# Performance work log

Hardware: AMD Instinct MI355X
Metric: run time of the kernel (lower is better)

Reference implementation:

```python
import jax, jax.numpy as jnp
import numpy as np

N = 50000      # nodes
E = 800000     # edges (avg degree 16)
C_IN = 128
C_HID = 256
C_OUT = 256
SLOPE = 0.2    # LeakyReLU negative slope (PyG GATv2Conv default)


def gatv2_layer(x, src, dst, edge_attr, Wl, Wr, We, att, bias):
    """PyG GATv2Conv, heads=1, share_weights=False.
    e_ij = att . leaky_relu(Wl x_j + Wr x_i + We e_ij); softmax over incoming
    edges of each target i; out_i = sum_j alpha_ij * (Wl x_j) + bias."""
    xl = x @ Wl                       # [N, out] source transform
    xr = x @ Wr                       # [N, out] target transform
    ee = edge_attr[:, None] @ We      # [E, out] edge feature transform (edge_dim=1)
    m = xl[src] + xr[dst] + ee        # [E, out] per-edge message pre-activation
    e = jnp.einsum('ed,d->e', jax.nn.leaky_relu(m, SLOPE), att)  # [E]
    # segment softmax over target nodes
    emax = jax.ops.segment_max(e, dst, num_segments=N)           # [N]
    ex = jnp.exp(e - emax[dst])                                  # [E]
    denom = jax.ops.segment_sum(ex, dst, num_segments=N)         # [N]
    alpha = ex / denom[dst]                                      # [E]
    out = jax.ops.segment_sum(xl[src] * alpha[:, None], dst, num_segments=N)
    return out + bias


def setup_inputs() -> dict:
    key = jax.random.key(0)
    ks = jax.random.split(key, 24)

    def lin(k, i, o):
        return (jax.random.normal(k, (i, o), jnp.float32) / np.sqrt(i)).astype(jnp.float32)

    inp = {
        'features': jax.random.normal(ks[0], (N, C_IN), jnp.float32),
        'edge_index': jax.random.randint(ks[1], (2, E), 0, N, dtype=jnp.int64),
        'edge_attr': jax.random.uniform(ks[2], (E,), jnp.float32),
        # conv1: c_in -> c_hidden
        'Wl1': lin(ks[3], C_IN, C_HID), 'Wr1': lin(ks[4], C_IN, C_HID),
        'We1': lin(ks[5], 1, C_HID),
        'a1': jax.random.normal(ks[6], (C_HID,), jnp.float32) / np.sqrt(C_HID),
        'bb1': jnp.zeros((C_HID,), jnp.float32),
        # conv2: c_hidden -> c_hidden
        'Wl2': lin(ks[7], C_HID, C_HID), 'Wr2': lin(ks[8], C_HID, C_HID),
        'We2': lin(ks[9], 1, C_HID),
        'a2': jax.random.normal(ks[10], (C_HID,), jnp.float32) / np.sqrt(C_HID),
        'bb2': jnp.zeros((C_HID,), jnp.float32),
        # conv3: c_hidden -> c_out (concat=False, heads=1 -> same math)
        'Wl3': lin(ks[11], C_HID, C_OUT), 'Wr3': lin(ks[12], C_HID, C_OUT),
        'We3': lin(ks[13], 1, C_OUT),
        'a3': jax.random.normal(ks[14], (C_OUT,), jnp.float32) / np.sqrt(C_OUT),
        'bb3': jnp.zeros((C_OUT,), jnp.float32),
        # MLP head: Linear(c_out,10) -> relu -> Linear(10,1); dropout is eval-mode identity
        'Wh1': lin(ks[15], C_OUT, 10), 'bh1': jnp.zeros((10,), jnp.float32),
        'Wh2': lin(ks[16], 10, 1), 'bh2': jnp.zeros((1,), jnp.float32),
    }
    return inp


def reference(features, edge_index, edge_attr,
              Wl1, Wr1, We1, a1, bb1,
              Wl2, Wr2, We2, a2, bb2,
              Wl3, Wr3, We3, a3, bb3,
              Wh1, bh1, Wh2, bh2):
    src, dst = edge_index[0], edge_index[1]
    x1 = jax.nn.relu(gatv2_layer(features, src, dst, edge_attr, Wl1, Wr1, We1, a1, bb1))
    x2 = jax.nn.relu(gatv2_layer(x1, src, dst, edge_attr, Wl2, Wr2, We2, a2, bb2))
    x3 = jax.nn.relu(gatv2_layer(x2, src, dst, edge_attr, Wl3, Wr3, We3, a3, bb3))
    x4 = jnp.max(x3, axis=-2)                 # global max pool over nodes -> [c_out]
    x5 = jax.nn.relu(x4 @ Wh1 + bh1)          # [10]
    return x5 @ Wh2 + bh2                     # [1]
```

## Files before the change

kernel.cpp:

```cpp
#include <hip/hip_runtime.h>
#include <cstddef>
#include <cstdint>

typedef __attribute__((ext_vector_type(8))) short short8v;
typedef __attribute__((ext_vector_type(4))) short short4v;
typedef __attribute__((ext_vector_type(4))) float floatx4;

__device__ __forceinline__ float b2f(short u){
    return __uint_as_float(((unsigned)(unsigned short)u) << 16);
}
__device__ __forceinline__ short f2b(float f){
    unsigned x = __float_as_uint(f);
    unsigned r = x + 0x7FFFu + ((x >> 16) & 1u);
    return (short)(r >> 16);
}
__device__ __forceinline__ float loadF(const void* p, size_t i, int isBf16){
    return isBf16 ? b2f(((const short*)p)[i]) : ((const float*)p)[i];
}
__device__ __forceinline__ int loadI(const void* p, size_t i, int isI64){
    return isI64 ? ((const int*)p)[2 * i] : ((const int*)p)[i];
}

__global__ void detect_kernel(const void* feat, const void* ei, int E, int* flags){
    int lane = threadIdx.x;
    if (lane >= 8 && lane < 16) flags[lane] = 0;
    const unsigned short* fs = (const unsigned short*)feat;
    int plaus = 0;
    for (int j = lane; j < 128; j += 64){
        unsigned short s = fs[2 * j];
        int e = (s >> 7) & 0xFF;
        if (s == 0 || (e >= 100 && e <= 140)) plaus++;
    }
    #pragma unroll
    for (int o = 32; o > 0; o >>= 1) plaus += __shfl_xor(plaus, o);
    const int* ew = (const int*)ei;
    int zeros = 0;
    for (int j = lane; j < 128; j += 64) if (ew[2 * j + 1] == 0) zeros++;
    #pragma unroll
    for (int o = 32; o > 0; o >>= 1) zeros += __shfl_xor(zeros, o);
    if (lane == 0){ flags[0] = (plaus >= 64) ? 1 : 0; flags[1] = (zeros >= 64) ? 1 : 0; }
    (void)E;
}

__global__ void sentinel_kernel(void* out, const int* flags, float v){
    if (threadIdx.x == 0){
        if (flags[0]) ((short*)out)[0] = f2b(v);
        else          ((float*)out)[0] = v;
    }
}

__global__ void zero3(int* cnt, int* fill, unsigned* pool, int N){
    int i = blockIdx.x * 256 + threadIdx.x;
    if (i < N){ cnt[i] = 0; fill[i] = 0; }
    if (i < 256) pool[i] = 0u;
}

__global__ void hist_kernel(const void* __restrict__ ei, int* __restrict__ cnt, int E,
                            const int* __restrict__ flags){
    int i = blockIdx.x * 256 + threadIdx.x;
    if (i < E) atomicAdd(&cnt[loadI(ei, (size_t)E + i, flags[1])], 1);
}

__global__ void scanA(const int* __restrict__ cnt, int* __restrict__ off,
                      int* __restrict__ partial, int N){
    __shared__ int wsum[16];
    const int t = threadIdx.x, w = t >> 6, lane = t & 63;
    int i = blockIdx.x * 1024 + t;
    int v = (i < N) ? cnt[i] : 0;
    int x = v;
    #pragma unroll
    for (int o = 1; o < 64; o <<= 1){
        int y = __shfl_up(x, o);
        if (lane >= o) x += y;
    }
    if (lane == 63) wsum[w] = x;
    __syncthreads();
    if (w == 0){
        int mv = (lane < 16) ? wsum[lane] : 0;
        int xx = mv;
        #pragma unroll
        for (int o = 1; o < 16; o <<= 1){
            int y = __shfl_up(xx, o);
            if (lane >= o) xx += y;
        }
        if (lane < 16) wsum[lane] = xx - mv;
    }
    __syncthreads();
    int incl = x + wsum[w];
    if (i < N) off[i] = incl - v;
    if (t == 1023) partial[blockIdx.x] = incl;
}

__global__ void scanB(int* __restrict__ partial, int* __restrict__ off, int nb, int N){
    int lane = threadIdx.x;
    int v = (lane < nb) ? partial[lane] : 0;
    int x = v;
    #pragma unroll
    for (int o = 1; o < 64; o <<= 1){
        int y = __shfl_up(x, o);
        if (lane >= o) x += y;
    }
    if (lane < nb) partial[lane] = x - v;
    if (lane == 63) off[N] = x;
}

__global__ void scanC(int* __restrict__ off, const int* __restrict__ partial, int N){
    int i = blockIdx.x * 1024 + threadIdx.x;
    if (i < N) off[i] += partial[blockIdx.x];
}

__global__ void scatter_kernel(const void* __restrict__ ei, const void* __restrict__ ea,
                               const int* __restrict__ off, int* __restrict__ fill,
                               int* __restrict__ srcS, float* __restrict__ eaS,
                               int E, const int* __restrict__ flags){
    int i = blockIdx.x * 256 + threadIdx.x;
    if (i >= E) return;
    int d = loadI(ei, (size_t)E + i, flags[1]);
    int pos = off[d] + atomicAdd(&fill[d], 1);
    srcS[pos] = loadI(ei, (size_t)i, flags[1]);
    eaS[pos] = loadF(ea, (size_t)i, flags[0]);
}

__global__ void prep_b(const void* __restrict__ W, short* __restrict__ bhi,
                       short* __restrict__ blo, int K, const int* __restrict__ flags,
                       int* __restrict__ hasLo){
    int idx = blockIdx.x * 256 + threadIdx.x;
    int k = idx >> 8, c = idx & 255;
    float v = loadF(W, idx, flags[0]);
    short h = f2b(v);
    short l = f2b(v - b2f(h));
    bhi[(size_t)c * K + k] = h;
    blo[(size_t)c * K + k] = l;
    if (__ballot(l != 0) != 0ull && (threadIdx.x & 63) == 0) atomicOr(hasLo, 1);
}

struct DJob { const void* src; float* dst; int n; };
struct DJobs { DJob j[13]; };
__global__ void decode_many(DJobs jobs, const int* __restrict__ flags){
    const DJob J = jobs.j[blockIdx.x];
    int fbf = flags[0];
    for (int i = threadIdx.x; i < J.n; i += 256)
        J.dst[i] = loadF(J.src, (size_t)i, fbf);
}

template<int BZ>
__global__ __launch_bounds__(256, 3) void gemm_tpl(
        const void* __restrict__ A, const short* __restrict__ Alo, int aRaw,
        const short* __restrict__ Bhi, const short* __restrict__ Blo,
        float* __restrict__ C, int M, int K,
        const int* __restrict__ flags, const int* __restrict__ bLoFlag){
    if (BZ ? (bLoFlag[0] != 0) : (bLoFlag[0] == 0)) return;
    __shared__ __align__(16) short Ah[128 * 64];
    __shared__ __align__(16) short Al[128 * 64];
    __shared__ __align__(16) short Bh[128 * 64];
    __shared__ __align__(16) short Bl[BZ ? 8 : 128 * 64];
    const int fbf = flags[0];
    const int az = (aRaw && fbf) ? 1 : 0;
    const int t = threadIdx.x;
    const int w = t >> 6, lane = t & 63;
    const int wr = w >> 1, wc = w & 1;
    const int bRow = blockIdx.x * 128;
    const int bCol = blockIdx.y * 128;

    floatx4 acc[4][4];
    #pragma unroll
    for (int m = 0; m < 4; m++)
        #pragma unroll
        for (int n = 0; n < 4; n++) acc[m][n] = (floatx4){0.f, 0.f, 0.f, 0.f};

    for (int k0 = 0; k0 < K; k0 += 64){
        #pragma unroll
        for (int i = 0; i < 4; i++){
            int e = i * 256 + t;
            int r = e >> 3, c = e & 7;
            int sw = (((c << 4) ^ ((r & 7) << 4)) >> 1);
            int gr = bRow + r; if (gr >= M) gr = M - 1;
            size_t ga = (size_t)gr * K + k0 + c * 8;
            if (aRaw){
                if (fbf){
                    *(short8v*)&Ah[r * 64 + sw] = *(const short8v*)&((const short*)A)[ga];
                } else {
                    const float* Af = (const float*)A;
                    floatx4 v0 = *(const floatx4*)&Af[ga];
                    floatx4 v1 = *(const floatx4*)&Af[ga + 4];
                    short8v h, l;
                    #pragma unroll
                    for (int j = 0; j < 4; j++){
                        short hj = f2b(v0[j]);
                        h[j] = hj; l[j] = f2b(v0[j] - b2f(hj));
                        short hk = f2b(v1[j]);
                        h[4 + j] = hk; l[4 + j] = f2b(v1[j] - b2f(hk));
                    }
                    *(short8v*)&Ah[r * 64 + sw] = h;
                    *(short8v*)&Al[r * 64 + sw] = l;
                }
            } else {
                *(short8v*)&Ah[r * 64 + sw] = *(const short8v*)&((const short*)A)[ga];
                *(short8v*)&Al[r * 64 + sw] = *(const short8v*)&Alo[ga];
            }
            size_t gb = (size_t)(bCol + r) * K + k0 + c * 8;
            *(short8v*)&Bh[r * 64 + sw] = *(const short8v*)&Bhi[gb];
            if (!BZ) *(short8v*)&Bl[r * 64 + sw] = *(const short8v*)&Blo[gb];
        }
        __syncthreads();
        #pragma unroll
        for (int ks = 0; ks < 2; ks++){
            short8v a_h[4], a_l[4], b_h[4], b_l[4];
            #pragma unroll
            for (int m = 0; m < 4; m++){
                int ar = wr * 64 + m * 16 + (lane & 15);
                int co = (((ks * 64 + ((lane >> 4) << 4)) ^ ((ar & 7) << 4)) >> 1);
                a_h[m] = *(const short8v*)&Ah[ar * 64 + co];
                if (!az) a_l[m] = *(const short8v*)&Al[ar * 64 + co];
            }
            #pragma unroll
            for (int n = 0; n < 4; n++){
                int br = wc * 64 + n * 16 + (lane & 15);
                int co = (((ks * 64 + ((lane >> 4) << 4)) ^ ((br & 7) << 4)) >> 1);
                b_h[n] = *(const short8v*)&Bh[br * 64 + co];
                if (!BZ) b_l[n] = *(const short8v*)&Bl[br * 64 + co];
            }
            #pragma unroll
            for (int m = 0; m < 4; m++)
                #pragma unroll
                for (int n = 0; n < 4; n++){
                    if (!az) acc[m][n] = __builtin_amdgcn_mfma_f32_16x16x32_bf16(
                                             a_l[m], b_h[n], acc[m][n], 0, 0, 0);
                    if (!BZ) acc[m][n] = __builtin_amdgcn_mfma_f32_16x16x32_bf16(
                                             a_h[m], b_l[n], acc[m][n], 0, 0, 0);
                    acc[m][n] = __builtin_amdgcn_mfma_f32_16x16x32_bf16(
                                    a_h[m], b_h[n], acc[m][n], 0, 0, 0);
                }
        }
        __syncthreads();
    }
    #pragma unroll
    for (int m = 0; m < 4; m++){
        int rb = bRow + wr * 64 + m * 16 + ((lane >> 4) << 2);
        #pragma unroll
        for (int n = 0; n < 4; n++){
            int cg = bCol + wc * 64 + n * 16 + (lane & 15);
            #pragma unroll
            for (int r = 0; r < 4; r++){
                int gr = rb + r;
                if (gr < M) C[(size_t)gr * 512 + cg] = acc[m][n][r];
            }
        }
    }
}

__global__ __launch_bounds__(256) void fused_agg(const float* __restrict__ PR,
        const int* __restrict__ srcS, const float* __restrict__ eaS,
        const int* __restrict__ off, const float* __restrict__ WeF,
        const float* __restrict__ attF, const float* __restrict__ bbF,
        short* __restrict__ QHi, short* __restrict__ QLo, int N){
    int node = blockIdx.x * 4 + (threadIdx.x >> 6);
    int lane = threadIdx.x & 63;
    if (node >= N) return;
    const int beg = off[node], end = off[node + 1];
    const int dd = lane << 2;
    const floatx4 xr4 = *(const floatx4*)&PR[(size_t)node * 512 + 256 + dd];
    const floatx4 we4 = *(const floatx4*)&WeF[dd];
    const floatx4 at4 = *(const floatx4*)&attF[dd];
    float m = -1e30f, ssum = 0.f;
    floatx4 a4 = (floatx4){0.f, 0.f, 0.f, 0.f};
    for (int k0 = beg; k0 < end; k0 += 8){
        floatx4 v[8]; float pp[8]; float eav[8];
        #pragma unroll
        for (int c = 0; c < 8; c++){
            int k = k0 + c; if (k >= end) k = end - 1;
            int s = srcS[k];
            eav[c] = eaS[k];
            v[c] = *(const floatx4*)&PR[(size_t)s * 512 + dd];
        }
        #pragma unroll
        for (int c = 0; c < 8; c++){
            float p = 0.f;
            #pragma unroll
            for (int j = 0; j < 4; j++){
                float tv = v[c][j] + xr4[j] + eav[c] * we4[j];
                tv = tv > 0.f ? tv : 0.2f * tv;
                p += tv * at4[j];
            }
            #pragma unroll
            for (int o = 32; o > 0; o >>= 1) p += __shfl_xor(p, o);
            pp[c] = (k0 + c < end) ? p : -1e30f;
        }
        float pm = pp[0];
        #pragma unroll
        for (int c = 1; c < 8; c++) pm = fmaxf(pm, pp[c]);
        float newm = fmaxf(m, pm);
        float scale = __expf(m - newm);
        ssum *= scale;
        a4[0] *= scale; a4[1] *= scale; a4[2] *= scale; a4[3] *= scale;
        #pragma unroll
        for (int c = 0; c < 8; c++){
            float wgt = __expf(pp[c] - newm);
            ssum += wgt;
            a4[0] += wgt * v[c][0]; a4[1] += wgt * v[c][1];
            a4[2] += wgt * v[c][2]; a4[3] += wgt * v[c][3];
        }
        m = newm;
    }
    float inv = (end > beg) ? 1.f / ssum : 0.f;
    short4v h4, l4;
    #pragma unroll
    for (int j = 0; j < 4; j++){
        float o = fmaxf(a4[j] * inv + bbF[dd + j], 0.f);
        short h = f2b(o);
        h4[j] = h;
        l4[j] = f2b(o - b2f(h));
    }
    *(short4v*)&QHi[(size_t)node * 256 + dd] = h4;
    *(short4v*)&QLo[(size_t)node * 256 + dd] = l4;
}

__global__ __launch_bounds__(256) void col_max2(const short* __restrict__ hi,
        const short* __restrict__ lo, unsigned* __restrict__ pool, int N){
    int lane = threadIdx.x & 63;
    int w = threadIdx.x >> 6;
    int dd = lane << 2;
    floatx4 mx = (floatx4){0.f, 0.f, 0.f, 0.f};
    for (int r = blockIdx.x * 4 + w; r < N; r += gridDim.x * 4){
        short4v h = *(const short4v*)&hi[(size_t)r * 256 + dd];
        short4v l = *(const short4v*)&lo[(size_t)r * 256 + dd];
        mx[0] = fmaxf(mx[0], b2f(h[0]) + b2f(l[0]));
        mx[1] = fmaxf(mx[1], b2f(h[1]) + b2f(l[1]));
        mx[2] = fmaxf(mx[2], b2f(h[2]) + b2f(l[2]));
        mx[3] = fmaxf(mx[3], b2f(h[3]) + b2f(l[3]));
    }
    atomicMax(&pool[dd + 0], __float_as_uint(mx[0]));
    atomicMax(&pool[dd + 1], __float_as_uint(mx[1]));
    atomicMax(&pool[dd + 2], __float_as_uint(mx[2]));
    atomicMax(&pool[dd + 3], __float_as_uint(mx[3]));
}

__global__ void head_kernel(const unsigned* __restrict__ pool, const float* __restrict__ Wh1F,
        const float* __restrict__ bh1F, const float* __restrict__ Wh2F,
        const float* __restrict__ bh2F, void* __restrict__ out, const int* __restrict__ flags){
    int lane = threadIdx.x;
    float acc = 0.f;
    if (lane < 10){
        acc = bh1F[lane];
        for (int d = 0; d < 256; ++d)
            acc += __uint_as_float(pool[d]) * Wh1F[d * 10 + lane];
        acc = fmaxf(acc, 0.f) * Wh2F[lane];
    }
    #pragma unroll
    for (int o = 32; o > 0; o >>= 1) acc += __shfl_xor(acc, o);
    if (lane == 0){
        float r = acc + bh2F[0];
        if (flags[0]) ((short*)out)[0] = f2b(r);
        else          ((float*)out)[0] = r;
    }
}

extern "C" void kernel_launch(void* const* d_in, const int* in_sizes, int n_in,
                              void* d_out, int out_size, void* d_ws, size_t ws_size,
                              hipStream_t stream){
    const void* feat = d_in[0];
    const void* ei   = d_in[1];
    const void* ea   = d_in[2];
    const void* Wl[3] = {d_in[3], d_in[8],  d_in[13]};
    const void* Wr[3] = {d_in[4], d_in[9],  d_in[14]};
    const void* We[3] = {d_in[5], d_in[10], d_in[15]};
    const void* at[3] = {d_in[6], d_in[11], d_in[16]};
    const void* bb[3] = {d_in[7], d_in[12], d_in[17]};
    const void* Wh1 = d_in[18];
    const void* bh1 = d_in[19];
    const void* Wh2 = d_in[20];
    const void* bh2 = d_in[21];

    const int N = in_sizes[0] / 128;
    const int E = in_sizes[1] / 2;
    const int Kin[3] = {128, 256, 256};
    const int nb = (N + 1023) / 1024;

    char* p = (char*)d_ws;
    auto alloc = [&](size_t bytes) -> void* {
        void* r = (void*)p; p += (bytes + 255) & ~(size_t)255; return r;
    };
    int*   flags   = (int*)alloc(256);
    int*   partial = (int*)alloc(256 * 4);
    int*   off   = (int*)alloc((size_t)(N + 1) * 4);
    int*   cnt   = (int*)alloc((size_t)N * 4);
    int*   fill  = (int*)alloc((size_t)N * 4);
    int*   srcS  = (int*)alloc((size_t)E * 4);
    float* eaS   = (float*)alloc((size_t)E * 4);
    float* PR    = (float*)alloc((size_t)N * 512 * 4);
    short* QHi   = (short*)alloc((size_t)N * 256 * 2);
    short* QLo   = (short*)alloc((size_t)N * 256 * 2);
    short* BtH[3]; short* BtL[3];
    for (int i = 0; i < 3; i++){
        BtH[i] = (short*)alloc((size_t)512 * Kin[i] * 2);
        BtL[i] = (short*)alloc((size_t)512 * Kin[i] * 2);
    }
    float* WeF  = (float*)alloc(3 * 256 * 4);
    float* attF = (float*)alloc(3 * 256 * 4);
    float* bbF  = (float*)alloc(3 * 256 * 4);
    float* Wh1F = (float*)alloc(2560 * 4);
    float* bh1F = (float*)alloc(16 * 4);
    float* Wh2F = (float*)alloc(16 * 4);
    float* bh2F = (float*)alloc(4 * 4);
    unsigned* pool = (unsigned*)alloc(256 * 4);
    size_t need = (size_t)(p - (char*)d_ws);

    detect_kernel<<<dim3(1), dim3(64), 0, stream>>>(feat, ei, E, flags);
    sentinel_kernel<<<dim3(1), dim3(1), 0, stream>>>(d_out, flags, 777.0f);
    if (need > ws_size){
        sentinel_kernel<<<dim3(1), dim3(1), 0, stream>>>(d_out, flags, 555.0f);
        return;
    }

    zero3<<<dim3((N + 255) / 256), dim3(256), 0, stream>>>(cnt, fill, pool, N);
    hist_kernel<<<dim3((E + 255) / 256), dim3(256), 0, stream>>>(ei, cnt, E, flags);
    scanA<<<dim3(nb), dim3(1024), 0, stream>>>(cnt, off, partial, N);
    scanB<<<dim3(1), dim3(64), 0, stream>>>(partial, off, nb, N);
    scanC<<<dim3(nb), dim3(1024), 0, stream>>>(off, partial, N);
    scatter_kernel<<<dim3((E + 255) / 256), dim3(256), 0, stream>>>(ei, ea, off, fill,
                                                                    srcS, eaS, E, flags);
    for (int i = 0; i < 3; i++){
        prep_b<<<dim3(Kin[i]), dim3(256), 0, stream>>>(Wl[i], BtH[i], BtL[i],
                                                       Kin[i], flags, &flags[8 + i]);
        prep_b<<<dim3(Kin[i]), dim3(256), 0, stream>>>(Wr[i], BtH[i] + (size_t)256 * Kin[i],
                                                       BtL[i] + (size_t)256 * Kin[i],
                                                       Kin[i], flags, &flags[8 + i]);
    }
    DJobs jobs;
    for (int i = 0; i < 3; i++){
        jobs.j[i]     = { We[i], WeF  + i * 256, 256 };
        jobs.j[3 + i] = { at[i], attF + i * 256, 256 };
        jobs.j[6 + i] = { bb[i], bbF  + i * 256, 256 };
    }
    jobs.j[9]  = { Wh1, Wh1F, 2560 };
    jobs.j[10] = { bh1, bh1F, 10 };
    jobs.j[11] = { Wh2, Wh2F, 10 };
    jobs.j[12] = { bh2, bh2F, 1 };
    decode_many<<<dim3(13), dim3(256), 0, stream>>>(jobs, flags);

    dim3 gemm_grid((N + 127) / 128, 4);
    for (int L = 0; L < 3; L++){
        const void* A = (L == 0) ? feat : (const void*)QHi;
        int aRaw = (L == 0) ? 1 : 0;
        gemm_tpl<1><<<gemm_grid, dim3(256), 0, stream>>>(A, QLo, aRaw, BtH[L], BtL[L],
                                                         PR, N, Kin[L], flags, &flags[8 + L]);
        gemm_tpl<0><<<gemm_grid, dim3(256), 0, stream>>>(A, QLo, aRaw, BtH[L], BtL[L],
                                                         PR, N, Kin[L], flags, &flags[8 + L]);
        fused_agg<<<dim3((N + 3) / 4), dim3(256), 0, stream>>>(PR, srcS, eaS, off,
                                                               WeF + L * 256, attF + L * 256,
                                                               bbF + L * 256, QHi, QLo, N);
    }
    col_max2<<<dim3(256), dim3(256), 0, stream>>>(QHi, QLo, pool, N);
    head_kernel<<<dim3(1), dim3(64), 0, stream>>>(pool, Wh1F, bh1F, Wh2F, bh2F, d_out, flags);
    (void)n_in; (void)out_size;
}
```

Measured before the change: 861.5 us.

## Use direct global-to-LDS loads in GEMM and pack edge src/attr pairs

```diff
diff --git a/kernel.cpp b/kernel.cpp
--- a/kernel.cpp
+++ b/kernel.cpp
@@ -19,6 +19,11 @@
 }
 __device__ __forceinline__ int loadI(const void* p, size_t i, int isI64){
     return isI64 ? ((const int*)p)[2 * i] : ((const int*)p)[i];
+}
+__device__ __forceinline__ void gload16(const void* g, void* l){
+    __builtin_amdgcn_global_load_lds(
+        (const __attribute__((address_space(1))) void*)g,
+        (__attribute__((address_space(3))) void*)l, 16, 0, 0);
 }
 
 __global__ void detect_kernel(const void* feat, const void* ei, int E, int* flags){
@@ -111,14 +116,15 @@
 
 __global__ void scatter_kernel(const void* __restrict__ ei, const void* __restrict__ ea,
                                const int* __restrict__ off, int* __restrict__ fill,
-                               int* __restrict__ srcS, float* __restrict__ eaS,
-                               int E, const int* __restrict__ flags){
+                               int2* __restrict__ se, int E, const int* __restrict__ flags){
     int i = blockIdx.x * 256 + threadIdx.x;
     if (i >= E) return;
     int d = loadI(ei, (size_t)E + i, flags[1]);
     int pos = off[d] + atomicAdd(&fill[d], 1);
-    srcS[pos] = loadI(ei, (size_t)i, flags[1]);
-    eaS[pos] = loadF(ea, (size_t)i, flags[0]);
+    int2 q;
+    q.x = loadI(ei, (size_t)i, flags[1]);
+    q.y = __float_as_int(loadF(ea, (size_t)i, flags[0]));
+    se[pos] = q;
 }
 
 __global__ void prep_b(const void* __restrict__ W, short* __restrict__ bhi,
@@ -156,11 +162,13 @@
     __shared__ __align__(16) short Bl[BZ ? 8 : 128 * 64];
     const int fbf = flags[0];
     const int az = (aRaw && fbf) ? 1 : 0;
+    const int aF32 = (aRaw && !fbf) ? 1 : 0;
     const int t = threadIdx.x;
     const int w = t >> 6, lane = t & 63;
     const int wr = w >> 1, wc = w & 1;
     const int bRow = blockIdx.x * 128;
     const int bCol = blockIdx.y * 128;
+    const short* Ahp = (const short*)A;
 
     floatx4 acc[4][4];
     #pragma unroll
@@ -170,37 +178,43 @@
 
     for (int k0 = 0; k0 < K; k0 += 64){
         #pragma unroll
-        for (int i = 0; i < 4; i++){
-            int e = i * 256 + t;
-            int r = e >> 3, c = e & 7;
-            int sw = (((c << 4) ^ ((r & 7) << 4)) >> 1);
-            int gr = bRow + r; if (gr >= M) gr = M - 1;
-            size_t ga = (size_t)gr * K + k0 + c * 8;
-            if (aRaw){
-                if (fbf){
-                    *(short8v*)&Ah[r * 64 + sw] = *(const short8v*)&((const short*)A)[ga];
-                } else {
-                    const float* Af = (const float*)A;
-                    floatx4 v0 = *(const floatx4*)&Af[ga];
-                    floatx4 v1 = *(const floatx4*)&Af[ga + 4];
-                    short8v h, l;
-                    #pragma unroll
-                    for (int j = 0; j < 4; j++){
-                        short hj = f2b(v0[j]);
-                        h[j] = hj; l[j] = f2b(v0[j] - b2f(hj));
-                        short hk = f2b(v1[j]);
-                        h[4 + j] = hk; l[4 + j] = f2b(v1[j] - b2f(hk));
-                    }
-                    *(short8v*)&Ah[r * 64 + sw] = h;
-                    *(short8v*)&Al[r * 64 + sw] = l;
+        for (int ps = 0; ps < 4; ps++){
+            int seg = ps * 4 + w;
+            int row = seg * 8 + (lane >> 3);
+            int cl  = lane & 7;
+            int cg  = cl ^ (row & 7);
+            int gr = bRow + row; if (gr >= M) gr = M - 1;
+            size_t ga = (size_t)gr * K + k0 + cg * 8;
+            if (!aF32){
+                gload16(&Ahp[ga], &Ah[seg * 512]);
+                if (!az) gload16(&Alo[ga], &Al[seg * 512]);
+            }
+            size_t gb = (size_t)(bCol + row) * K + k0 + cg * 8;
+            gload16(&Bhi[gb], &Bh[seg * 512]);
+            if (!BZ) gload16(&Blo[gb], &Bl[seg * 512]);
+        }
+        if (aF32){
+            #pragma unroll
+            for (int i = 0; i < 4; i++){
+                int e = i * 256 + t;
+                int r = e >> 3, c = e & 7;
+                int sw = ((c ^ (r & 7)) << 3);
+                int gr = bRow + r; if (gr >= M) gr = M - 1;
+                size_t ga = (size_t)gr * K + k0 + c * 8;
+                const float* Af = (const float*)A;
+                floatx4 v0 = *(const floatx4*)&Af[ga];
+                floatx4 v1 = *(const floatx4*)&Af[ga + 4];
+                short8v h, l;
+                #pragma unroll
+                for (int j = 0; j < 4; j++){
+                    short hj = f2b(v0[j]);
+                    h[j] = hj; l[j] = f2b(v0[j] - b2f(hj));
+                    short hk = f2b(v1[j]);
+                    h[4 + j] = hk; l[4 + j] = f2b(v1[j] - b2f(hk));
                 }
-            } else {
-                *(short8v*)&Ah[r * 64 + sw] = *(const short8v*)&((const short*)A)[ga];
-                *(short8v*)&Al[r * 64 + sw] = *(const short8v*)&Alo[ga];
-            }
-            size_t gb = (size_t)(bCol + r) * K + k0 + c * 8;
-            *(short8v*)&Bh[r * 64 + sw] = *(const short8v*)&Bhi[gb];
-            if (!BZ) *(short8v*)&Bl[r * 64 + sw] = *(const short8v*)&Blo[gb];
+                *(short8v*)&Ah[r * 64 + sw] = h;
+                *(short8v*)&Al[r * 64 + sw] = l;
+            }
         }
         __syncthreads();
         #pragma unroll
@@ -250,9 +264,9 @@
 }
 
 __global__ __launch_bounds__(256) void fused_agg(const float* __restrict__ PR,
-        const int* __restrict__ srcS, const float* __restrict__ eaS,
-        const int* __restrict__ off, const float* __restrict__ WeF,
-        const float* __restrict__ attF, const float* __restrict__ bbF,
+        const int2* __restrict__ se, const int* __restrict__ off,
+        const float* __restrict__ WeF, const float* __restrict__ attF,
+        const float* __restrict__ bbF,
         short* __restrict__ QHi, short* __restrict__ QLo, int N){
     int node = blockIdx.x * 4 + (threadIdx.x >> 6);
     int lane = threadIdx.x & 63;
@@ -269,9 +283,9 @@
         #pragma unroll
         for (int c = 0; c < 8; c++){
             int k = k0 + c; if (k >= end) k = end - 1;
-            int s = srcS[k];
-            eav[c] = eaS[k];
-            v[c] = *(const floatx4*)&PR[(size_t)s * 512 + dd];
+            int2 q = se[k];
+            eav[c] = __int_as_float(q.y);
+            v[c] = *(const floatx4*)&PR[(size_t)q.x * 512 + dd];
         }
         #pragma unroll
         for (int c = 0; c < 8; c++){
@@ -289,18 +303,20 @@
         float pm = pp[0];
         #pragma unroll
         for (int c = 1; c < 8; c++) pm = fmaxf(pm, pp[c]);
-        float newm = fmaxf(m, pm);
-        float scale = __expf(m - newm);
-        ssum *= scale;
-        a4[0] *= scale; a4[1] *= scale; a4[2] *= scale; a4[3] *= scale;
+        if (pm > m){
+            float newm = pm;
+            float scale = __expf(m - newm);
+            ssum *= scale;
+            a4[0] *= scale; a4[1] *= scale; a4[2] *= scale; a4[3] *= scale;
+            m = newm;
+        }
         #pragma unroll
         for (int c = 0; c < 8; c++){
-            float wgt = __expf(pp[c] - newm);
+            float wgt = __expf(pp[c] - m);
             ssum += wgt;
             a4[0] += wgt * v[c][0]; a4[1] += wgt * v[c][1];
             a4[2] += wgt * v[c][2]; a4[3] += wgt * v[c][3];
         }
-        m = newm;
     }
     float inv = (end > beg) ? 1.f / ssum : 0.f;
     short4v h4, l4;
@@ -385,8 +401,7 @@
     int*   off   = (int*)alloc((size_t)(N + 1) * 4);
     int*   cnt   = (int*)alloc((size_t)N * 4);
     int*   fill  = (int*)alloc((size_t)N * 4);
-    int*   srcS  = (int*)alloc((size_t)E * 4);
-    float* eaS   = (float*)alloc((size_t)E * 4);
+    int2*  se    = (int2*)alloc((size_t)E * 8);
     float* PR    = (float*)alloc((size_t)N * 512 * 4);
     short* QHi   = (short*)alloc((size_t)N * 256 * 2);
     short* QLo   = (short*)alloc((size_t)N * 256 * 2);
@@ -418,7 +433,7 @@
     scanB<<<dim3(1), dim3(64), 0, stream>>>(partial, off, nb, N);
     scanC<<<dim3(nb), dim3(1024), 0, stream>>>(off, partial, N);
     scatter_kernel<<<dim3((E + 255) / 256), dim3(256), 0, stream>>>(ei, ea, off, fill,
-                                                                    srcS, eaS, E, flags);
+                                                                    se, E, flags);
     for (int i = 0; i < 3; i++){
         prep_b<<<dim3(Kin[i]), dim3(256), 0, stream>>>(Wl[i], BtH[i], BtL[i],
                                                        Kin[i], flags, &flags[8 + i]);
@@ -446,7 +461,7 @@
                                                          PR, N, Kin[L], flags, &flags[8 + L]);
         gemm_tpl<0><<<gemm_grid, dim3(256), 0, stream>>>(A, QLo, aRaw, BtH[L], BtL[L],
                                                          PR, N, Kin[L], flags, &flags[8 + L]);
-        fused_agg<<<dim3((N + 3) / 4), dim3(256), 0, stream>>>(PR, srcS, eaS, off,
+        fused_agg<<<dim3((N + 3) / 4), dim3(256), 0, stream>>>(PR, se, off,
                                                                WeF + L * 256, attF + L * 256,
                                                                bbF + L * 256, QHi, QLo, N);
     }
```

Measured after the change: 858.2 us. No clear change (-0.4%).

## Double-buffer GEMM tiles with direct global-to-LDS async loads

Applied to the files above, without the earlier changes.

```diff
diff --git a/kernel.cpp b/kernel.cpp
--- a/kernel.cpp
+++ b/kernel.cpp
@@ -19,6 +19,11 @@
 }
 __device__ __forceinline__ int loadI(const void* p, size_t i, int isI64){
     return isI64 ? ((const int*)p)[2 * i] : ((const int*)p)[i];
+}
+__device__ __forceinline__ void gload16(const void* g, void* l){
+    __builtin_amdgcn_global_load_lds(
+        (const __attribute__((address_space(1))) void*)g,
+        (__attribute__((address_space(3))) void*)l, 16, 0, 0);
 }
 
 __global__ void detect_kernel(const void* feat, const void* ei, int E, int* flags){
@@ -150,17 +155,20 @@
         float* __restrict__ C, int M, int K,
         const int* __restrict__ flags, const int* __restrict__ bLoFlag){
     if (BZ ? (bLoFlag[0] != 0) : (bLoFlag[0] == 0)) return;
-    __shared__ __align__(16) short Ah[128 * 64];
-    __shared__ __align__(16) short Al[128 * 64];
-    __shared__ __align__(16) short Bh[128 * 64];
-    __shared__ __align__(16) short Bl[BZ ? 8 : 128 * 64];
+    __shared__ __align__(16) short Ah[2][128 * 32];
+    __shared__ __align__(16) short Al[2][128 * 32];
+    __shared__ __align__(16) short Bh[2][128 * 32];
+    __shared__ __align__(16) short Bl[2][BZ ? 8 : 128 * 32];
     const int fbf = flags[0];
-    const int az = (aRaw && fbf) ? 1 : 0;
+    const int az   = (aRaw && fbf) ? 1 : 0;
+    const int aF32 = (aRaw && !fbf) ? 1 : 0;
     const int t = threadIdx.x;
     const int w = t >> 6, lane = t & 63;
     const int wr = w >> 1, wc = w & 1;
     const int bRow = blockIdx.x * 128;
     const int bCol = blockIdx.y * 128;
+    const short* Ahp = (const short*)A;
+    const float* Af  = (const float*)A;
 
     floatx4 acc[4][4];
     #pragma unroll
@@ -168,71 +176,92 @@
         #pragma unroll
         for (int n = 0; n < 4; n++) acc[m][n] = (floatx4){0.f, 0.f, 0.f, 0.f};
 
-    for (int k0 = 0; k0 < K; k0 += 64){
-        #pragma unroll
-        for (int i = 0; i < 4; i++){
-            int e = i * 256 + t;
-            int r = e >> 3, c = e & 7;
-            int sw = (((c << 4) ^ ((r & 7) << 4)) >> 1);
-            int gr = bRow + r; if (gr >= M) gr = M - 1;
-            size_t ga = (size_t)gr * K + k0 + c * 8;
-            if (aRaw){
-                if (fbf){
-                    *(short8v*)&Ah[r * 64 + sw] = *(const short8v*)&((const short*)A)[ga];
-                } else {
-                    const float* Af = (const float*)A;
-                    floatx4 v0 = *(const floatx4*)&Af[ga];
-                    floatx4 v1 = *(const floatx4*)&Af[ga + 4];
-                    short8v h, l;
-                    #pragma unroll
-                    for (int j = 0; j < 4; j++){
-                        short hj = f2b(v0[j]);
-                        h[j] = hj; l[j] = f2b(v0[j] - b2f(hj));
-                        short hk = f2b(v1[j]);
-                        h[4 + j] = hk; l[4 + j] = f2b(v1[j] - b2f(hk));
-                    }
-                    *(short8v*)&Ah[r * 64 + sw] = h;
-                    *(short8v*)&Al[r * 64 + sw] = l;
+    auto STAGE = [&](int buf, int kk){
+        #pragma unroll
+        for (int iss = 0; iss < 2; iss++){
+            int ci  = (iss * 4 + w) * 64 + lane;
+            int row = ci >> 2;
+            int cg  = (ci & 3) ^ (row & 3);
+            int gr = bRow + row; if (gr >= M) gr = M - 1;
+            size_t ga  = (size_t)gr * K + kk + cg * 8;
+            size_t gbi = (size_t)(bCol + row) * K + kk + cg * 8;
+            int seg = (iss * 4 + w) * 512;
+            if (!aF32){
+                gload16(&Ahp[ga], &Ah[buf][seg]);
+                if (!az) gload16(&Alo[ga], &Al[buf][seg]);
+            }
+            gload16(&Bhi[gbi], &Bh[buf][seg]);
+            if (!BZ) gload16(&Blo[gbi], &Bl[buf][seg]);
+        }
+        if (aF32){
+            #pragma unroll
+            for (int iss = 0; iss < 2; iss++){
+                int ci  = (iss * 4 + w) * 64 + lane;
+                int row = ci >> 2, cl = ci & 3;
+                int slot = cl ^ (row & 3);
+                int gr = bRow + row; if (gr >= M) gr = M - 1;
+                size_t ga = (size_t)gr * K + kk + cl * 8;
+                floatx4 v0 = *(const floatx4*)&Af[ga];
+                floatx4 v1 = *(const floatx4*)&Af[ga + 4];
+                short8v h, l;
+                #pragma unroll
+                for (int j = 0; j < 4; j++){
+                    short hj = f2b(v0[j]);
+                    h[j] = hj; l[j] = f2b(v0[j] - b2f(hj));
+                    short hk = f2b(v1[j]);
+                    h[4 + j] = hk; l[4 + j] = f2b(v1[j] - b2f(hk));
                 }
-            } else {
-                *(short8v*)&Ah[r * 64 + sw] = *(const short8v*)&((const short*)A)[ga];
-                *(short8v*)&Al[r * 64 + sw] = *(const short8v*)&Alo[ga];
+                *(short8v*)&Ah[buf][row * 32 + slot * 8] = h;
+                *(short8v*)&Al[buf][row * 32 + slot * 8] = l;
             }
-            size_t gb = (size_t)(bCol + r) * K + k0 + c * 8;
-            *(short8v*)&Bh[r * 64 + sw] = *(const short8v*)&Bhi[gb];
-            if (!BZ) *(short8v*)&Bl[r * 64 + sw] = *(const short8v*)&Blo[gb];
-        }
-        __syncthreads();
-        #pragma unroll
-        for (int ks = 0; ks < 2; ks++){
-            short8v a_h[4], a_l[4], b_h[4], b_l[4];
-            #pragma unroll
-            for (int m = 0; m < 4; m++){
-                int ar = wr * 64 + m * 16 + (lane & 15);
-                int co = (((ks * 64 + ((lane >> 4) << 4)) ^ ((ar & 7) << 4)) >> 1);
-                a_h[m] = *(const short8v*)&Ah[ar * 64 + co];
-                if (!az) a_l[m] = *(const short8v*)&Al[ar * 64 + co];
-            }
+        }
+    };
+
+    const int T = K >> 5;
+    STAGE(0, 0);
+    int cur = 0;
+    for (int kt = 0; kt < T; ++kt){
+        if (kt + 1 < T) STAGE(cur ^ 1, (kt + 1) << 5);
+        if (aF32){
+            asm volatile("s_waitcnt vmcnt(0) lgkmcnt(0)" ::: "memory");
+        } else if (kt + 1 >= T){
+            asm volatile("s_waitcnt vmcnt(0)" ::: "memory");
+        } else if (az){
+            if (BZ) asm volatile("s_waitcnt vmcnt(4)" ::: "memory");
+            else    asm volatile("s_waitcnt vmcnt(6)" ::: "memory");
+        } else {
+            if (BZ) asm volatile("s_waitcnt vmcnt(6)" ::: "memory");
+            else    asm volatile("s_waitcnt vmcnt(8)" ::: "memory");
+        }
+        __builtin_amdgcn_s_barrier();
+        short8v a_h[4], a_l[4], b_h[4], b_l[4];
+        #pragma unroll
+        for (int m = 0; m < 4; m++){
+            int ar = wr * 64 + m * 16 + (lane & 15);
+            int co = (((lane >> 4) ^ (ar & 3)) << 3);
+            a_h[m] = *(const short8v*)&Ah[cur][ar * 32 + co];
+            if (!az) a_l[m] = *(const short8v*)&Al[cur][ar * 32 + co];
+        }
+        #pragma unroll
+        for (int n = 0; n < 4; n++){
+            int br = wc * 64 + n * 16 + (lane & 15);
+            int co = (((lane >> 4) ^ (br & 3)) << 3);
+            b_h[n] = *(const short8v*)&Bh[cur][br * 32 + co];
+            if (!BZ) b_l[n] = *(const short8v*)&Bl[cur][br * 32 + co];
+        }
+        #pragma unroll
+        for (int m = 0; m < 4; m++)
             #pragma unroll
             for (int n = 0; n < 4; n++){
-                int br = wc * 64 + n * 16 + (lane & 15);
-                int co = (((ks * 64 + ((lane >> 4) << 4)) ^ ((br & 7) << 4)) >> 1);
-                b_h[n] = *(const short8v*)&Bh[br * 64 + co];
-                if (!BZ) b_l[n] = *(const short8v*)&Bl[br * 64 + co];
+                if (!az) acc[m][n] = __builtin_amdgcn_mfma_f32_16x16x32_bf16(
+                                         a_l[m], b_h[n], acc[m][n], 0, 0, 0);
+                if (!BZ) acc[m][n] = __builtin_amdgcn_mfma_f32_16x16x32_bf16(
+                                         a_h[m], b_l[n], acc[m][n], 0, 0, 0);
+                acc[m][n] = __builtin_amdgcn_mfma_f32_16x16x32_bf16(
+                                a_h[m], b_h[n], acc[m][n], 0, 0, 0);
             }
-            #pragma unroll
-            for (int m = 0; m < 4; m++)
-                #pragma unroll
-                for (int n = 0; n < 4; n++){
-                    if (!az) acc[m][n] = __builtin_amdgcn_mfma_f32_16x16x32_bf16(
-                                             a_l[m], b_h[n], acc[m][n], 0, 0, 0);
-                    if (!BZ) acc[m][n] = __builtin_amdgcn_mfma_f32_16x16x32_bf16(
-                                             a_h[m], b_l[n], acc[m][n], 0, 0, 0);
-                    acc[m][n] = __builtin_amdgcn_mfma_f32_16x16x32_bf16(
-                                    a_h[m], b_h[n], acc[m][n], 0, 0, 0);
-                }
-        }
-        __syncthreads();
+        __builtin_amdgcn_s_barrier();
+        cur ^= 1;
     }
     #pragma unroll
     for (int m = 0; m < 4; m++){
```

Measured after the change: 826.2 us. 1.04x faster.

## Load GEMM operands directly from global memory and merge setup/prep launches

Applied to the files above, without the earlier changes.

```diff
diff --git a/kernel.cpp b/kernel.cpp
--- a/kernel.cpp
+++ b/kernel.cpp
@@ -21,25 +21,40 @@
     return isI64 ? ((const int*)p)[2 * i] : ((const int*)p)[i];
 }
 
-__global__ void detect_kernel(const void* feat, const void* ei, int E, int* flags){
-    int lane = threadIdx.x;
-    if (lane >= 8 && lane < 16) flags[lane] = 0;
-    const unsigned short* fs = (const unsigned short*)feat;
-    int plaus = 0;
-    for (int j = lane; j < 128; j += 64){
-        unsigned short s = fs[2 * j];
-        int e = (s >> 7) & 0xFF;
-        if (s == 0 || (e >= 100 && e <= 140)) plaus++;
-    }
-    #pragma unroll
-    for (int o = 32; o > 0; o >>= 1) plaus += __shfl_xor(plaus, o);
-    const int* ew = (const int*)ei;
-    int zeros = 0;
-    for (int j = lane; j < 128; j += 64) if (ew[2 * j + 1] == 0) zeros++;
-    #pragma unroll
-    for (int o = 32; o > 0; o >>= 1) zeros += __shfl_xor(zeros, o);
-    if (lane == 0){ flags[0] = (plaus >= 64) ? 1 : 0; flags[1] = (zeros >= 64) ? 1 : 0; }
-    (void)E;
+__global__ void setup_kernel(const void* feat, const void* ei, int N, int* flags,
+                             int* cnt, int* fill, unsigned* pool, void* out){
+    int gid = blockIdx.x * 256 + threadIdx.x;
+    if (gid < N){ cnt[gid] = 0; fill[gid] = 0; }
+    if (gid < 256) pool[gid] = 0u;
+    if (blockIdx.x == 0){
+        int t = threadIdx.x;
+        if (t < 64){
+            if (t >= 8 && t < 16) flags[t] = 0;
+            const unsigned short* fs = (const unsigned short*)feat;
+            int plaus = 0;
+            for (int j = t; j < 128; j += 64){
+                unsigned short s = fs[2 * j];
+                int e = (s >> 7) & 0xFF;
+                if (s == 0 || (e >= 100 && e <= 140)) plaus++;
+            }
+            #pragma unroll
+            for (int o = 32; o > 0; o >>= 1) plaus += __shfl_xor(plaus, o);
+            const int* ew = (const int*)ei;
+            int zeros = 0;
+            for (int j = t; j < 128; j += 64) if (ew[2 * j + 1] == 0) zeros++;
+            #pragma unroll
+            for (int o = 32; o > 0; o >>= 1) zeros += __shfl_xor(zeros, o);
+            if (t == 0){
+                flags[0] = (plaus >= 64) ? 1 : 0;
+                flags[1] = (zeros >= 64) ? 1 : 0;
+            }
+        }
+        __syncthreads();
+        if (threadIdx.x == 0){
+            if (flags[0]) ((short*)out)[0] = f2b(777.0f);
+            else          ((float*)out)[0] = 777.0f;
+        }
+    }
 }
 
 __global__ void sentinel_kernel(void* out, const int* flags, float v){
@@ -47,12 +62,6 @@
         if (flags[0]) ((short*)out)[0] = f2b(v);
         else          ((float*)out)[0] = v;
     }
-}
-
-__global__ void zero3(int* cnt, int* fill, unsigned* pool, int N){
-    int i = blockIdx.x * 256 + threadIdx.x;
-    if (i < N){ cnt[i] = 0; fill[i] = 0; }
-    if (i < 256) pool[i] = 0u;
 }
 
 __global__ void hist_kernel(const void* __restrict__ ei, int* __restrict__ cnt, int E,
@@ -121,17 +130,19 @@
     eaS[pos] = loadF(ea, (size_t)i, flags[0]);
 }
 
-__global__ void prep_b(const void* __restrict__ W, short* __restrict__ bhi,
-                       short* __restrict__ blo, int K, const int* __restrict__ flags,
-                       int* __restrict__ hasLo){
+struct PJobs { const void* W[6]; short* bhi[6]; short* blo[6]; int K[6]; int fidx[6]; };
+__global__ void prep_all(PJobs J, int* __restrict__ flags){
+    int j = blockIdx.y;
+    int K = J.K[j];
+    if (blockIdx.x >= K) return;
     int idx = blockIdx.x * 256 + threadIdx.x;
     int k = idx >> 8, c = idx & 255;
-    float v = loadF(W, idx, flags[0]);
+    float v = loadF(J.W[j], idx, flags[0]);
     short h = f2b(v);
     short l = f2b(v - b2f(h));
-    bhi[(size_t)c * K + k] = h;
-    blo[(size_t)c * K + k] = l;
-    if (__ballot(l != 0) != 0ull && (threadIdx.x & 63) == 0) atomicOr(hasLo, 1);
+    J.bhi[j][(size_t)c * K + k] = h;
+    J.blo[j][(size_t)c * K + k] = l;
+    if (__ballot(l != 0) != 0ull && (threadIdx.x & 63) == 0) atomicOr(&flags[J.fidx[j]], 1);
 }
 
 struct DJob { const void* src; float* dst; int n; };
@@ -144,99 +155,108 @@
 }
 
 template<int BZ>
-__global__ __launch_bounds__(256, 3) void gemm_tpl(
+__global__ __launch_bounds__(512) void gemm_direct(
         const void* __restrict__ A, const short* __restrict__ Alo, int aRaw,
         const short* __restrict__ Bhi, const short* __restrict__ Blo,
         float* __restrict__ C, int M, int K,
         const int* __restrict__ flags, const int* __restrict__ bLoFlag){
     if (BZ ? (bLoFlag[0] != 0) : (bLoFlag[0] == 0)) return;
-    __shared__ __align__(16) short Ah[128 * 64];
-    __shared__ __align__(16) short Al[128 * 64];
-    __shared__ __align__(16) short Bh[128 * 64];
-    __shared__ __align__(16) short Bl[BZ ? 8 : 128 * 64];
     const int fbf = flags[0];
-    const int az = (aRaw && fbf) ? 1 : 0;
+    const int az   = (aRaw && fbf) ? 1 : 0;
+    const int aF32 = (aRaw && !fbf) ? 1 : 0;
     const int t = threadIdx.x;
     const int w = t >> 6, lane = t & 63;
     const int wr = w >> 1, wc = w & 1;
     const int bRow = blockIdx.x * 128;
     const int bCol = blockIdx.y * 128;
-
-    floatx4 acc[4][4];
-    #pragma unroll
-    for (int m = 0; m < 4; m++)
+    const short* Ahp = (const short*)A;
+    const float* Af  = (const float*)A;
+
+    floatx4 acc[2][4];
+    #pragma unroll
+    for (int m = 0; m < 2; m++)
         #pragma unroll
         for (int n = 0; n < 4; n++) acc[m][n] = (floatx4){0.f, 0.f, 0.f, 0.f};
 
-    for (int k0 = 0; k0 < K; k0 += 64){
-        #pragma unroll
-        for (int i = 0; i < 4; i++){
-            int e = i * 256 + t;
-            int r = e >> 3, c = e & 7;
-            int sw = (((c << 4) ^ ((r & 7) << 4)) >> 1);
-            int gr = bRow + r; if (gr >= M) gr = M - 1;
-            size_t ga = (size_t)gr * K + k0 + c * 8;
-            if (aRaw){
-                if (fbf){
-                    *(short8v*)&Ah[r * 64 + sw] = *(const short8v*)&((const short*)A)[ga];
-                } else {
-                    const float* Af = (const float*)A;
-                    floatx4 v0 = *(const floatx4*)&Af[ga];
-                    floatx4 v1 = *(const floatx4*)&Af[ga + 4];
-                    short8v h, l;
-                    #pragma unroll
-                    for (int j = 0; j < 4; j++){
-                        short hj = f2b(v0[j]);
-                        h[j] = hj; l[j] = f2b(v0[j] - b2f(hj));
-                        short hk = f2b(v1[j]);
-                        h[4 + j] = hk; l[4 + j] = f2b(v1[j] - b2f(hk));
-                    }
-                    *(short8v*)&Ah[r * 64 + sw] = h;
-                    *(short8v*)&Al[r * 64 + sw] = l;
-                }
-            } else {
-                *(short8v*)&Ah[r * 64 + sw] = *(const short8v*)&((const short*)A)[ga];
-                *(short8v*)&Al[r * 64 + sw] = *(const short8v*)&Alo[ga];
-            }
-            size_t gb = (size_t)(bCol + r) * K + k0 + c * 8;
-            *(short8v*)&Bh[r * 64 + sw] = *(const short8v*)&Bhi[gb];
-            if (!BZ) *(short8v*)&Bl[r * 64 + sw] = *(const short8v*)&Blo[gb];
-        }
-        __syncthreads();
-        #pragma unroll
-        for (int ks = 0; ks < 2; ks++){
-            short8v a_h[4], a_l[4], b_h[4], b_l[4];
-            #pragma unroll
-            for (int m = 0; m < 4; m++){
-                int ar = wr * 64 + m * 16 + (lane & 15);
-                int co = (((ks * 64 + ((lane >> 4) << 4)) ^ ((ar & 7) << 4)) >> 1);
-                a_h[m] = *(const short8v*)&Ah[ar * 64 + co];
-                if (!az) a_l[m] = *(const short8v*)&Al[ar * 64 + co];
-            }
-            #pragma unroll
-            for (int n = 0; n < 4; n++){
-                int br = wc * 64 + n * 16 + (lane & 15);
-                int co = (((ks * 64 + ((lane >> 4) << 4)) ^ ((br & 7) << 4)) >> 1);
-                b_h[n] = *(const short8v*)&Bh[br * 64 + co];
-                if (!BZ) b_l[n] = *(const short8v*)&Bl[br * 64 + co];
-            }
-            #pragma unroll
-            for (int m = 0; m < 4; m++)
+    const int kc = (lane >> 4) << 3;
+    size_t ga[2]; size_t gb[4];
+    #pragma unroll
+    for (int m = 0; m < 2; m++){
+        int gr = bRow + wr * 32 + m * 16 + (lane & 15);
+        if (gr >= M) gr = M - 1;
+        ga[m] = (size_t)gr * K + kc;
+    }
+    #pragma unroll
+    for (int n = 0; n < 4; n++)
+        gb[n] = (size_t)(bCol + wc * 64 + n * 16 + (lane & 15)) * K + kc;
+
+    const int T = K >> 5;
+    if (!aF32){
+        #pragma unroll 2
+        for (int kt = 0; kt < T; ++kt){
+            const int kk = kt << 5;
+            short8v a_h[2], a_l[2], b_h[4];
+            #pragma unroll
+            for (int m = 0; m < 2; m++){
+                a_h[m] = *(const short8v*)&Ahp[ga[m] + kk];
+                if (!az) a_l[m] = *(const short8v*)&Alo[ga[m] + kk];
+            }
+            #pragma unroll
+            for (int n = 0; n < 4; n++)
+                b_h[n] = *(const short8v*)&Bhi[gb[n] + kk];
+            #pragma unroll
+            for (int m = 0; m < 2; m++)
                 #pragma unroll
                 for (int n = 0; n < 4; n++){
                     if (!az) acc[m][n] = __builtin_amdgcn_mfma_f32_16x16x32_bf16(
                                              a_l[m], b_h[n], acc[m][n], 0, 0, 0);
-                    if (!BZ) acc[m][n] = __builtin_amdgcn_mfma_f32_16x16x32_bf16(
-                                             a_h[m], b_l[n], acc[m][n], 0, 0, 0);
+                    if (!BZ){
+                        short8v b_l = *(const short8v*)&Blo[gb[n] + kk];
+                        acc[m][n] = __builtin_amdgcn_mfma_f32_16x16x32_bf16(
+                                        a_h[m], b_l, acc[m][n], 0, 0, 0);
+                    }
                     acc[m][n] = __builtin_amdgcn_mfma_f32_16x16x32_bf16(
                                     a_h[m], b_h[n], acc[m][n], 0, 0, 0);
                 }
         }
-        __syncthreads();
-    }
-    #pragma unroll
-    for (int m = 0; m < 4; m++){
-        int rb = bRow + wr * 64 + m * 16 + ((lane >> 4) << 2);
+    } else {
+        for (int kt = 0; kt < T; ++kt){
+            const int kk = kt << 5;
+            short8v a_h[2], a_l[2], b_h[4];
+            #pragma unroll
+            for (int m = 0; m < 2; m++){
+                floatx4 v0 = *(const floatx4*)&Af[ga[m] + kk];
+                floatx4 v1 = *(const floatx4*)&Af[ga[m] + kk + 4];
+                #pragma unroll
+                for (int j = 0; j < 4; j++){
+                    short hj = f2b(v0[j]);
+                    a_h[m][j] = hj; a_l[m][j] = f2b(v0[j] - b2f(hj));
+                    short hk = f2b(v1[j]);
+                    a_h[m][4 + j] = hk; a_l[m][4 + j] = f2b(v1[j] - b2f(hk));
+                }
+            }
+            #pragma unroll
+            for (int n = 0; n < 4; n++)
+                b_h[n] = *(const short8v*)&Bhi[gb[n] + kk];
+            #pragma unroll
+            for (int m = 0; m < 2; m++)
+                #pragma unroll
+                for (int n = 0; n < 4; n++){
+                    acc[m][n] = __builtin_amdgcn_mfma_f32_16x16x32_bf16(
+                                    a_l[m], b_h[n], acc[m][n], 0, 0, 0);
+                    if (!BZ){
+                        short8v b_l = *(const short8v*)&Blo[gb[n] + kk];
+                        acc[m][n] = __builtin_amdgcn_mfma_f32_16x16x32_bf16(
+                                        a_h[m], b_l, acc[m][n], 0, 0, 0);
+                    }
+                    acc[m][n] = __builtin_amdgcn_mfma_f32_16x16x32_bf16(
+                                    a_h[m], b_h[n], acc[m][n], 0, 0, 0);
+                }
+        }
+    }
+    #pragma unroll
+    for (int m = 0; m < 2; m++){
+        int rb = bRow + wr * 32 + m * 16 + ((lane >> 4) << 2);
         #pragma unroll
         for (int n = 0; n < 4; n++){
             int cg = bCol + wc * 64 + n * 16 + (lane & 15);
@@ -405,27 +425,32 @@
     unsigned* pool = (unsigned*)alloc(256 * 4);
     size_t need = (size_t)(p - (char*)d_ws);
 
-    detect_kernel<<<dim3(1), dim3(64), 0, stream>>>(feat, ei, E, flags);
-    sentinel_kernel<<<dim3(1), dim3(1), 0, stream>>>(d_out, flags, 777.0f);
+    setup_kernel<<<dim3((N + 255) / 256), dim3(256), 0, stream>>>(feat, ei, N, flags,
+                                                                  cnt, fill, pool, d_out);
     if (need > ws_size){
         sentinel_kernel<<<dim3(1), dim3(1), 0, stream>>>(d_out, flags, 555.0f);
         return;
     }
 
-    zero3<<<dim3((N + 255) / 256), dim3(256), 0, stream>>>(cnt, fill, pool, N);
     hist_kernel<<<dim3((E + 255) / 256), dim3(256), 0, stream>>>(ei, cnt, E, flags);
     scanA<<<dim3(nb), dim3(1024), 0, stream>>>(cnt, off, partial, N);
     scanB<<<dim3(1), dim3(64), 0, stream>>>(partial, off, nb, N);
     scanC<<<dim3(nb), dim3(1024), 0, stream>>>(off, partial, N);
     scatter_kernel<<<dim3((E + 255) / 256), dim3(256), 0, stream>>>(ei, ea, off, fill,
                                                                     srcS, eaS, E, flags);
+    PJobs pj;
     for (int i = 0; i < 3; i++){
-        prep_b<<<dim3(Kin[i]), dim3(256), 0, stream>>>(Wl[i], BtH[i], BtL[i],
-                                                       Kin[i], flags, &flags[8 + i]);
-        prep_b<<<dim3(Kin[i]), dim3(256), 0, stream>>>(Wr[i], BtH[i] + (size_t)256 * Kin[i],
-                                                       BtL[i] + (size_t)256 * Kin[i],
-                                                       Kin[i], flags, &flags[8 + i]);
-    }
+        pj.W[2 * i]     = Wl[i];
+        pj.bhi[2 * i]   = BtH[i];
+        pj.blo[2 * i]   = BtL[i];
+        pj.W[2 * i + 1]   = Wr[i];
+        pj.bhi[2 * i + 1] = BtH[i] + (size_t)256 * Kin[i];
+        pj.blo[2 * i + 1] = BtL[i] + (size_t)256 * Kin[i];
+        pj.K[2 * i] = pj.K[2 * i + 1] = Kin[i];
+        pj.fidx[2 * i] = pj.fidx[2 * i + 1] = 8 + i;
+    }
+    prep_all<<<dim3(256, 6), dim3(256), 0, stream>>>(pj, flags);
+
     DJobs jobs;
     for (int i = 0; i < 3; i++){
         jobs.j[i]     = { We[i], WeF  + i * 256, 256 };
@@ -442,10 +467,10 @@
     for (int L = 0; L < 3; L++){
         const void* A = (L == 0) ? feat : (const void*)QHi;
         int aRaw = (L == 0) ? 1 : 0;
-        gemm_tpl<1><<<gemm_grid, dim3(256), 0, stream>>>(A, QLo, aRaw, BtH[L], BtL[L],
-                                                         PR, N, Kin[L], flags, &flags[8 + L]);
-        gemm_tpl<0><<<gemm_grid, dim3(256), 0, stream>>>(A, QLo, aRaw, BtH[L], BtL[L],
-                                                         PR, N, Kin[L], flags, &flags[8 + L]);
+        gemm_direct<1><<<gemm_grid, dim3(512), 0, stream>>>(A, QLo, aRaw, BtH[L], BtL[L],
+                                                            PR, N, Kin[L], flags, &flags[8 + L]);
+        gemm_direct<0><<<gemm_grid, dim3(512), 0, stream>>>(A, QLo, aRaw, BtH[L], BtL[L],
+                                                            PR, N, Kin[L], flags, &flags[8 + L]);
         fused_agg<<<dim3((N + 3) / 4), dim3(256), 0, stream>>>(PR, srcS, eaS, off,
                                                                WeF + L * 256, attF + L * 256,
                                                                bbF + L * 256, QHi, QLo, N);
```

New measurement: 1.040 ms. +20.8%, slower.
